# Kernel tuning notes

Hardware: AMD Instinct MI355X
Metric: run time of the kernel (lower is better)

## Reference

```python
import jax, jax.numpy as jnp
import numpy as np

B, S, D, H = 2, 2048, 1024, 16
HSZ = D // H  # 64


def setup_inputs() -> dict:
    key = jax.random.key(0)
    k0, k1, k2, k3, k4 = jax.random.split(key, 5)
    scale = 0.02
    return {
        "x": jax.random.normal(k0, (B, S, D), dtype=jnp.float32),
        "in_proj_w": jax.random.normal(k1, (3 * D, D), dtype=jnp.float32) * scale,
        "in_proj_b": jax.random.normal(k2, (3 * D,), dtype=jnp.float32) * scale,
        "out_proj_w": jax.random.normal(k3, (D, D), dtype=jnp.float32) * scale,
        "out_proj_b": jax.random.normal(k4, (D,), dtype=jnp.float32) * scale,
    }


def reference(x, in_proj_w, in_proj_b, out_proj_w, out_proj_b):
    # Packed QKV projection (self-attention fast path: query is key is value).
    qkv = x @ in_proj_w.T + in_proj_b              # (B, S, 3D)
    q, k, v = jnp.split(qkv, 3, axis=-1)           # each (B, S, D)

    def to_heads(t):
        return t.reshape(B, S, H, HSZ).transpose(0, 2, 1, 3)  # (B, H, S, hsz)

    q, k, v = to_heads(q), to_heads(k), to_heads(v)

    # Causal additive bias: -inf above the diagonal (tril keeps, logical_not masks).
    neg_inf = jnp.float32(-jnp.inf)
    causal = jnp.tril(jnp.ones((S, S), dtype=bool))
    attn_bias = jnp.where(causal, jnp.float32(0.0), neg_inf)  # (S, S)

    inv_sqrt = jnp.float32(1.0 / np.sqrt(HSZ))
    scores = jnp.einsum("bhqd,bhkd->bhqk", q * inv_sqrt, k) + attn_bias
    attn_w = jax.nn.softmax(scores, axis=-1)       # (B, H, S, S)

    out = jnp.einsum("bhqk,bhkd->bhqd", attn_w, v)  # (B, H, S, hsz)
    out = jnp.nan_to_num(out, nan=0.0)              # matches torch.nan_to_num_
    out = out.transpose(0, 2, 1, 3).reshape(B, S, D)  # concat heads
    out = out @ out_proj_w.T + out_proj_b           # (B, S, D)
    return out, attn_w
```

## Files before the change

kernel.cpp:

```cpp
#include <hip/hip_runtime.h>
#include <stdint.h>

typedef __bf16 bf16;
typedef __attribute__((ext_vector_type(8))) __bf16 bf16x8;
typedef __attribute__((ext_vector_type(4))) __bf16 bf16x4;
typedef __attribute__((ext_vector_type(4))) float f32x4;

#define MFMA16(a, b, c) __builtin_amdgcn_mfma_f32_16x16x32_bf16((a), (b), (c), 0, 0, 0)

constexpr int S = 2048, Dm = 1024, HS = 64;
constexpr float SCALE = 0.125f;
constexpr float SHIFT = 8.0f;

__device__ __forceinline__ int ktmax_of(int qt) { return (qt * 64 + 191) >> 7; }

__device__ __forceinline__ void job_decode(int j, int& qt, int& kg) {
  int acc = 0;
  for (int q = 0; q < 32; ++q) {
    const int ng = (ktmax_of(q) + 3) >> 2;
    if (j < acc + ng) { qt = q; kg = j - acc; return; }
    acc += ng;
  }
  qt = 31; kg = 0;
}

__device__ __forceinline__ void gld_lds16(const void* g, void* lds_uniform) {
  __builtin_amdgcn_global_load_lds(
      (const __attribute__((address_space(1))) void*)g,
      (__attribute__((address_space(3))) void*)lds_uniform,
      16, 0, 0);
}

__global__ __launch_bounds__(256) void cvt_kernel(const float* __restrict__ src,
                                                  bf16* __restrict__ dst, int n) {
  int i4 = (blockIdx.x * 256 + threadIdx.x) * 4;
  if (i4 < n) {
    const float4 f = *(const float4*)(src + i4);
    bf16x4 o;
    o[0] = (bf16)f.x; o[1] = (bf16)f.y; o[2] = (bf16)f.z; o[3] = (bf16)f.w;
    *(bf16x4*)(dst + i4) = o;
  }
}

__global__ __launch_bounds__(256) void gemm_bt_kernel(
    const bf16* __restrict__ A, const bf16* __restrict__ Bw,
    const float* __restrict__ bias, void* __restrict__ Cout,
    int N, int K, int out_is_bf16) {
  __shared__ bf16 As[128 * 32];
  __shared__ bf16 Bs[128 * 32];
  const int t = threadIdx.x;
  const int wave = t >> 6, lane = t & 63, quad = lane >> 4, l15 = lane & 15;
  const int wm = wave >> 1, wn = wave & 1;
  const int m0 = blockIdx.y * 128, n0 = blockIdx.x * 128;

  f32x4 acc[4][4];
#pragma unroll
  for (int mt = 0; mt < 4; ++mt)
#pragma unroll
    for (int nt = 0; nt < 4; ++nt) acc[mt][nt] = f32x4{0.f, 0.f, 0.f, 0.f};

  const bf16* Ag = A + (size_t)(m0 + (t >> 2)) * K + (t & 3) * 8;
  const bf16* Bg = Bw + (size_t)(n0 + (t >> 2)) * K + (t & 3) * 8;
  char* AsB = (char*)As;
  char* BsB = (char*)Bs;
  const int woff = wave * 1024;

  for (int k0 = 0; k0 < K; k0 += 32) {
    __syncthreads();
    gld_lds16(Ag + k0, AsB + woff);
    gld_lds16(Ag + (size_t)64 * K + k0, AsB + 4096 + woff);
    gld_lds16(Bg + k0, BsB + woff);
    gld_lds16(Bg + (size_t)64 * K + k0, BsB + 4096 + woff);
    __syncthreads();
    bf16x8 af[4], bfr[4];
#pragma unroll
    for (int mt = 0; mt < 4; ++mt)
      af[mt] = *(const bf16x8*)(As + (wm * 64 + mt * 16 + l15) * 32 + quad * 8);
#pragma unroll
    for (int nt = 0; nt < 4; ++nt)
      bfr[nt] = *(const bf16x8*)(Bs + (wn * 64 + nt * 16 + l15) * 32 + quad * 8);
#pragma unroll
    for (int mt = 0; mt < 4; ++mt)
#pragma unroll
      for (int nt = 0; nt < 4; ++nt)
        acc[mt][nt] = MFMA16(af[mt], bfr[nt], acc[mt][nt]);
  }

#pragma unroll
  for (int mt = 0; mt < 4; ++mt) {
    const int row = m0 + wm * 64 + mt * 16 + quad * 4;
#pragma unroll
    for (int nt = 0; nt < 4; ++nt) {
      const int col = n0 + wn * 64 + nt * 16 + l15;
      const float bcol = bias[col];
#pragma unroll
      for (int r = 0; r < 4; ++r) {
        float v = acc[mt][nt][r] + bcol;
        if (out_is_bf16)
          ((bf16*)Cout)[(size_t)(row + r) * N + col] = (bf16)v;
        else
          ((float*)Cout)[(size_t)(row + r) * N + col] = v;
      }
    }
  }
}

__global__ __launch_bounds__(256) void gemm_bt64_kernel(
    const bf16* __restrict__ A, const bf16* __restrict__ Bw,
    const float* __restrict__ bias, float* __restrict__ Cout,
    int N, int K) {
  __shared__ bf16 As[64 * 32];
  __shared__ bf16 Bs[128 * 32];
  const int t = threadIdx.x;
  const int wave = t >> 6, lane = t & 63, quad = lane >> 4, l15 = lane & 15;
  const int wm = wave >> 1, wn = wave & 1;
  const int m0 = blockIdx.y * 64, n0 = blockIdx.x * 128;

  f32x4 acc[2][4];
#pragma unroll
  for (int mt = 0; mt < 2; ++mt)
#pragma unroll
    for (int nt = 0; nt < 4; ++nt) acc[mt][nt] = f32x4{0.f, 0.f, 0.f, 0.f};

  const bf16* Ag = A + (size_t)(m0 + (t >> 2)) * K + (t & 3) * 8;
  const bf16* Bg = Bw + (size_t)(n0 + (t >> 2)) * K + (t & 3) * 8;
  char* AsB = (char*)As;
  char* BsB = (char*)Bs;
  const int woff = wave * 1024;

  for (int k0 = 0; k0 < K; k0 += 32) {
    __syncthreads();
    gld_lds16(Ag + k0, AsB + woff);
    gld_lds16(Bg + k0, BsB + woff);
    gld_lds16(Bg + (size_t)64 * K + k0, BsB + 4096 + woff);
    __syncthreads();
    bf16x8 af[2], bfr[4];
#pragma unroll
    for (int mt = 0; mt < 2; ++mt)
      af[mt] = *(const bf16x8*)(As + (wm * 32 + mt * 16 + l15) * 32 + quad * 8);
#pragma unroll
    for (int nt = 0; nt < 4; ++nt)
      bfr[nt] = *(const bf16x8*)(Bs + (wn * 64 + nt * 16 + l15) * 32 + quad * 8);
#pragma unroll
    for (int mt = 0; mt < 2; ++mt)
#pragma unroll
      for (int nt = 0; nt < 4; ++nt)
        acc[mt][nt] = MFMA16(af[mt], bfr[nt], acc[mt][nt]);
  }

#pragma unroll
  for (int mt = 0; mt < 2; ++mt) {
    const int row = m0 + wm * 32 + mt * 16 + quad * 4;
#pragma unroll
    for (int nt = 0; nt < 4; ++nt) {
      const int col = n0 + wn * 64 + nt * 16 + l15;
      const float bcol = bias[col];
#pragma unroll
      for (int r = 0; r < 4; ++r)
        Cout[(size_t)(row + r) * N + col] = acc[mt][nt][r] + bcol;
    }
  }
}

__global__ __launch_bounds__(256) void stats_kernel(const bf16* __restrict__ qkv,
                                                    float* __restrict__ lsum) {
  const int t = threadIdx.x, wave = t >> 6, lane = t & 63, quad = lane >> 4, l15 = lane & 15;
  int qt, kg;
  job_decode(79 - blockIdx.x, qt, kg);
  const int bh = blockIdx.y, b = bh >> 4, h = bh & 15;
  const int q0 = qt * 64;

  const bf16* qbase = qkv + (size_t)b * S * (3 * Dm) + h * HS;
  const bf16* kbase = qbase + Dm;
  const bf16* qrow = qbase + (size_t)(q0 + wave * 16 + l15) * (3 * Dm);
  const bf16x8 qf0 = *(const bf16x8*)(qrow + quad * 8);
  const bf16x8 qf1 = *(const bf16x8*)(qrow + 32 + quad * 8);
  const int rowb = q0 + wave * 16 + quad * 4;

  const int kt0 = kg * 4, kt1 = min(kt0 + 4, ktmax_of(qt));
  float accr[4] = {0.f, 0.f, 0.f, 0.f};

  for (int kt = kt0; kt < kt1; ++kt) {
    const int kc0 = kt * 128;
    f32x4 sacc[8];
#pragma unroll
    for (int nt = 0; nt < 8; ++nt) sacc[nt] = f32x4{0.f, 0.f, 0.f, 0.f};
#pragma unroll
    for (int nt = 0; nt < 8; ++nt) {
      const bf16* krow = kbase + (size_t)(kc0 + nt * 16 + l15) * (3 * Dm);
      const bf16x8 kf0 = *(const bf16x8*)(krow + quad * 8);
      const bf16x8 kf1 = *(const bf16x8*)(krow + 32 + quad * 8);
      sacc[nt] = MFMA16(qf0, kf0, sacc[nt]);
      sacc[nt] = MFMA16(qf1, kf1, sacc[nt]);
    }
#pragma unroll
    for (int nt = 0; nt < 8; ++nt) {
      const int col = kc0 + nt * 16 + l15;
#pragma unroll
      for (int r = 0; r < 4; ++r) {
        if (col <= rowb + r) accr[r] += __expf(sacc[nt][r] * SCALE - SHIFT);
      }
    }
  }
#pragma unroll
  for (int r = 0; r < 4; ++r) {
    float v = accr[r];
#pragma unroll
    for (int off = 1; off < 16; off <<= 1) v += __shfl_xor(v, off, 16);
    if (l15 == 0) atomicAdd(&lsum[bh * S + rowb + r], v);
  }
}

__global__ __launch_bounds__(256) void write_pv_kernel(
    const bf16* __restrict__ qkv, const float* __restrict__ lsum,
    float* __restrict__ attnw, float* __restrict__ Oacc) {
  constexpr int PSF = 132;
  constexpr int VST = 136;
  __shared__ float Ps[64 * PSF];
  __shared__ bf16 Vt[64 * VST];
  const int t = threadIdx.x, wave = t >> 6, lane = t & 63, quad = lane >> 4, l15 = lane & 15;
  int qt, kg;
  job_decode(79 - blockIdx.x, qt, kg);
  const int bh = blockIdx.y, b = bh >> 4, h = bh & 15;
  const int q0 = qt * 64;

  const bf16* qbase = qkv + (size_t)b * S * (3 * Dm) + h * HS;
  const bf16* kbase = qbase + Dm;
  const bf16* vbase = qbase + 2 * Dm;
  const bf16* qrow = qbase + (size_t)(q0 + wave * 16 + l15) * (3 * Dm);
  const bf16x8 qf0 = *(const bf16x8*)(qrow + quad * 8);
  const bf16x8 qf1 = *(const bf16x8*)(qrow + 32 + quad * 8);
  const int rowb = q0 + wave * 16 + quad * 4;

  float rl[4];
#pragma unroll
  for (int r = 0; r < 4; ++r) rl[r] = 1.f / lsum[bh * S + rowb + r];

  f32x4 oacc[4];
#pragma unroll
  for (int nto = 0; nto < 4; ++nto) oacc[nto] = f32x4{0.f, 0.f, 0.f, 0.f};

  float* aw = attnw + ((size_t)bh * S + q0) * S;
  const int kt0 = kg * 4, kt1 = min(kt0 + 4, ktmax_of(qt));

  for (int kt = kt0; kt < kt1; ++kt) {
    const int kc0 = kt * 128;
    __syncthreads();
    {
      ushort* vt = (ushort*)Vt;
#pragma unroll
      for (int it = 0; it < 16; ++it) {
        const int idx = it * 512 + t * 2;
        const int key = idx >> 6, hd = idx & 63;
        const unsigned u =
            *(const unsigned*)(vbase + (size_t)(kc0 + key) * (3 * Dm) + hd);
        vt[hd * VST + key] = (ushort)(u & 0xffffu);
        vt[(hd + 1) * VST + key] = (ushort)(u >> 16);
      }
    }
    f32x4 sacc[8];
#pragma unroll
    for (int nt = 0; nt < 8; ++nt) sacc[nt] = f32x4{0.f, 0.f, 0.f, 0.f};
#pragma unroll
    for (int nt = 0; nt < 8; ++nt) {
      const bf16* krow = kbase + (size_t)(kc0 + nt * 16 + l15) * (3 * Dm);
      const bf16x8 kf0 = *(const bf16x8*)(krow + quad * 8);
      const bf16x8 kf1 = *(const bf16x8*)(krow + 32 + quad * 8);
      sacc[nt] = MFMA16(qf0, kf0, sacc[nt]);
      sacc[nt] = MFMA16(qf1, kf1, sacc[nt]);
    }
#pragma unroll
    for (int nt = 0; nt < 8; ++nt) {
      const int col = kc0 + nt * 16 + l15;
#pragma unroll
      for (int r = 0; r < 4; ++r) {
        const float p = (col <= rowb + r)
                            ? __expf(sacc[nt][r] * SCALE - SHIFT) * rl[r]
                            : 0.f;
        Ps[(wave * 16 + quad * 4 + r) * PSF + nt * 16 + l15] = p;
      }
    }
    __syncthreads();

#pragma unroll
    for (int i = 0; i < 8; ++i) {
      const int idx = i * 256 + lane * 4;
      const int row16 = idx >> 7, col = idx & 127;
      const f32x4 v = *(const f32x4*)(Ps + (wave * 16 + row16) * PSF + col);
      __builtin_nontemporal_store(
          v, (f32x4*)(aw + (size_t)(wave * 16 + row16) * S + kc0 + col));
    }

#pragma unroll
    for (int ks = 0; ks < 4; ++ks) {
      const float* prow = Ps + (wave * 16 + l15) * PSF + ks * 32 + quad * 8;
      const f32x4 p0 = *(const f32x4*)prow;
      const f32x4 p1 = *(const f32x4*)(prow + 4);
      bf16x8 pa;
#pragma unroll
      for (int j = 0; j < 4; ++j) { pa[j] = (bf16)p0[j]; pa[4 + j] = (bf16)p1[j]; }
#pragma unroll
      for (int nto = 0; nto < 4; ++nto) {
        const bf16x8 vb =
            *(const bf16x8*)(Vt + (nto * 16 + l15) * VST + ks * 32 + quad * 8);
        oacc[nto] = MFMA16(pa, vb, oacc[nto]);
      }
    }
  }

#pragma unroll
  for (int nto = 0; nto < 4; ++nto) {
    const int hd = nto * 16 + l15;
#pragma unroll
    for (int r = 0; r < 4; ++r) {
      atomicAdd(&Oacc[((size_t)bh * S + rowb + r) * 64 + hd], oacc[nto][r]);
    }
  }
}

__global__ __launch_bounds__(256) void zf_kernel(float* __restrict__ attnw) {
  const int t = threadIdx.x;
  const int qt = blockIdx.x, bh = blockIdx.y;
  const int c0 = ktmax_of(qt) * 128;
  const int nv = (S - c0) >> 2;
  if (nv <= 0) return;
  float* aw = attnw + ((size_t)bh * S + qt * 64) * S + c0;
  const f32x4 z = {0.f, 0.f, 0.f, 0.f};
  for (int rr = 0; rr < 64; ++rr) {
    float* rowp = aw + (size_t)rr * S;
    for (int cc = t; cc < nv; cc += 256)
      __builtin_nontemporal_store(z, (f32x4*)(rowp + cc * 4));
  }
}

__global__ __launch_bounds__(256) void ocvt_kernel(const float* __restrict__ Oacc,
                                                   bf16* __restrict__ ho) {
  const int i4 = (blockIdx.x * 256 + threadIdx.x) * 4;
  const int bh = i4 >> 17, rem = i4 & 131071;
  const int row = rem >> 6, hd = rem & 63;
  const int b = bh >> 4, h = bh & 15;
  const float4 f = *(const float4*)(Oacc + i4);
  bf16x4 o;
  o[0] = (bf16)f.x; o[1] = (bf16)f.y; o[2] = (bf16)f.z; o[3] = (bf16)f.w;
  *(bf16x4*)(ho + (size_t)(b * S + row) * Dm + h * HS + hd) = o;
}

extern "C" void kernel_launch(void* const* d_in, const int* in_sizes, int n_in,
                              void* d_out, int out_size, void* d_ws, size_t ws_size,
                              hipStream_t stream) {
  (void)in_sizes; (void)n_in; (void)out_size; (void)ws_size;
  const float* x = (const float*)d_in[0];
  const float* wi = (const float*)d_in[1];
  const float* bi = (const float*)d_in[2];
  const float* wo = (const float*)d_in[3];
  const float* bo = (const float*)d_in[4];

  char* ws = (char*)d_ws;
  bf16* qkv = (bf16*)(ws);
  bf16* ho = (bf16*)(ws + 25165824);
  float* lsum = (float*)(ws + 25165824);
  float* Oacc = (float*)(ws + 33554432);
  bf16* xb = (bf16*)(ws + 33554432);
  bf16* wib = (bf16*)(ws + 41943040);
  bf16* wob = (bf16*)(ws);

  float* out = (float*)d_out;
  float* attnw = out + (size_t)4194304;

  cvt_kernel<<<4096, 256, 0, stream>>>(x, xb, 4194304);
  cvt_kernel<<<3072, 256, 0, stream>>>(wi, wib, 3145728);
  gemm_bt_kernel<<<dim3(24, 32), 256, 0, stream>>>(xb, wib, bi, qkv, 3072, 1024, 1);
  hipMemsetAsync(Oacc, 0, 16777216, stream);
  hipMemsetAsync(lsum, 0, 262144, stream);
  stats_kernel<<<dim3(80, 32), 256, 0, stream>>>(qkv, lsum);
  write_pv_kernel<<<dim3(80, 32), 256, 0, stream>>>(qkv, lsum, attnw, Oacc);
  zf_kernel<<<dim3(32, 32), 256, 0, stream>>>(attnw);
  cvt_kernel<<<1024, 256, 0, stream>>>(wo, wob, 1048576);
  ocvt_kernel<<<4096, 256, 0, stream>>>(Oacc, ho);
  gemm_bt64_kernel<<<dim3(8, 64), 256, 0, stream>>>(ho, wob, bo, out, 1024, 1024);
}
```

Before: 845.0 us.

## Fuse stats, PV, zero-fill and output conversion into one attention kernel per query tile

Replaces the split-K stats and write/PV kernels, the zero-fill kernel, the fp32 O accumulator memsets and the output conversion kernel with one kernel. Each block owns a full 64-row query tile: it zero-fills the masked columns, computes the row sums over all key tiles, then writes probabilities and the PV product, storing bf16 head output directly. This removes the atomics, the memsets and several launches. In exchange the grid shrinks from 80x32 to 32x32 blocks, so work is unbalanced across causal tiles (up to 16 key tiles per block) and occupancy is lower.

```diff
diff --git a/kernel.cpp b/kernel.cpp
--- a/kernel.cpp
+++ b/kernel.cpp
@@ -13,16 +13,6 @@
 constexpr float SHIFT = 8.0f;
 
 __device__ __forceinline__ int ktmax_of(int qt) { return (qt * 64 + 191) >> 7; }
-
-__device__ __forceinline__ void job_decode(int j, int& qt, int& kg) {
-  int acc = 0;
-  for (int q = 0; q < 32; ++q) {
-    const int ng = (ktmax_of(q) + 3) >> 2;
-    if (j < acc + ng) { qt = q; kg = j - acc; return; }
-    acc += ng;
-  }
-  qt = 31; kg = 0;
-}
 
 __device__ __forceinline__ void gld_lds16(const void* g, void* lds_uniform) {
   __builtin_amdgcn_global_load_lds(
@@ -44,8 +34,8 @@
 
 __global__ __launch_bounds__(256) void gemm_bt_kernel(
     const bf16* __restrict__ A, const bf16* __restrict__ Bw,
-    const float* __restrict__ bias, void* __restrict__ Cout,
-    int N, int K, int out_is_bf16) {
+    const float* __restrict__ bias, bf16* __restrict__ Cout,
+    int N, int K) {
   __shared__ bf16 As[128 * 32];
   __shared__ bf16 Bs[128 * 32];
   const int t = threadIdx.x;
@@ -94,13 +84,8 @@
       const int col = n0 + wn * 64 + nt * 16 + l15;
       const float bcol = bias[col];
 #pragma unroll
-      for (int r = 0; r < 4; ++r) {
-        float v = acc[mt][nt][r] + bcol;
-        if (out_is_bf16)
-          ((bf16*)Cout)[(size_t)(row + r) * N + col] = (bf16)v;
-        else
-          ((float*)Cout)[(size_t)(row + r) * N + col] = v;
-      }
+      for (int r = 0; r < 4; ++r)
+        Cout[(size_t)(row + r) * N + col] = (bf16)(acc[mt][nt][r] + bcol);
     }
   }
 }
@@ -162,67 +147,18 @@
   }
 }
 
-__global__ __launch_bounds__(256) void stats_kernel(const bf16* __restrict__ qkv,
-                                                    float* __restrict__ lsum) {
-  const int t = threadIdx.x, wave = t >> 6, lane = t & 63, quad = lane >> 4, l15 = lane & 15;
-  int qt, kg;
-  job_decode(79 - blockIdx.x, qt, kg);
-  const int bh = blockIdx.y, b = bh >> 4, h = bh & 15;
-  const int q0 = qt * 64;
-
-  const bf16* qbase = qkv + (size_t)b * S * (3 * Dm) + h * HS;
-  const bf16* kbase = qbase + Dm;
-  const bf16* qrow = qbase + (size_t)(q0 + wave * 16 + l15) * (3 * Dm);
-  const bf16x8 qf0 = *(const bf16x8*)(qrow + quad * 8);
-  const bf16x8 qf1 = *(const bf16x8*)(qrow + 32 + quad * 8);
-  const int rowb = q0 + wave * 16 + quad * 4;
-
-  const int kt0 = kg * 4, kt1 = min(kt0 + 4, ktmax_of(qt));
-  float accr[4] = {0.f, 0.f, 0.f, 0.f};
-
-  for (int kt = kt0; kt < kt1; ++kt) {
-    const int kc0 = kt * 128;
-    f32x4 sacc[8];
-#pragma unroll
-    for (int nt = 0; nt < 8; ++nt) sacc[nt] = f32x4{0.f, 0.f, 0.f, 0.f};
-#pragma unroll
-    for (int nt = 0; nt < 8; ++nt) {
-      const bf16* krow = kbase + (size_t)(kc0 + nt * 16 + l15) * (3 * Dm);
-      const bf16x8 kf0 = *(const bf16x8*)(krow + quad * 8);
-      const bf16x8 kf1 = *(const bf16x8*)(krow + 32 + quad * 8);
-      sacc[nt] = MFMA16(qf0, kf0, sacc[nt]);
-      sacc[nt] = MFMA16(qf1, kf1, sacc[nt]);
-    }
-#pragma unroll
-    for (int nt = 0; nt < 8; ++nt) {
-      const int col = kc0 + nt * 16 + l15;
-#pragma unroll
-      for (int r = 0; r < 4; ++r) {
-        if (col <= rowb + r) accr[r] += __expf(sacc[nt][r] * SCALE - SHIFT);
-      }
-    }
-  }
-#pragma unroll
-  for (int r = 0; r < 4; ++r) {
-    float v = accr[r];
-#pragma unroll
-    for (int off = 1; off < 16; off <<= 1) v += __shfl_xor(v, off, 16);
-    if (l15 == 0) atomicAdd(&lsum[bh * S + rowb + r], v);
-  }
-}
-
-__global__ __launch_bounds__(256) void write_pv_kernel(
-    const bf16* __restrict__ qkv, const float* __restrict__ lsum,
-    float* __restrict__ attnw, float* __restrict__ Oacc) {
+__global__ __launch_bounds__(256) void attn_fused_kernel(
+    const bf16* __restrict__ qkv, float* __restrict__ attnw,
+    bf16* __restrict__ ho) {
   constexpr int PSF = 132;
   constexpr int VST = 136;
   __shared__ float Ps[64 * PSF];
   __shared__ bf16 Vt[64 * VST];
   const int t = threadIdx.x, wave = t >> 6, lane = t & 63, quad = lane >> 4, l15 = lane & 15;
-  int qt, kg;
-  job_decode(79 - blockIdx.x, qt, kg);
+  const int qt = 31 - blockIdx.x;
   const int bh = blockIdx.y, b = bh >> 4, h = bh & 15;
   const int q0 = qt * 64;
+  const int ktmax = ktmax_of(qt);
 
   const bf16* qbase = qkv + (size_t)b * S * (3 * Dm) + h * HS;
   const bf16* kbase = qbase + Dm;
@@ -232,18 +168,58 @@
   const bf16x8 qf1 = *(const bf16x8*)(qrow + 32 + quad * 8);
   const int rowb = q0 + wave * 16 + quad * 4;
 
+  float* aw = attnw + ((size_t)bh * S + q0) * S;
+
+  {
+    const int c0 = ktmax * 128;
+    const int nv = (S - c0) >> 2;
+    if (nv > 0) {
+      const f32x4 z = {0.f, 0.f, 0.f, 0.f};
+      for (int rr = 0; rr < 64; ++rr) {
+        float* rowp = aw + (size_t)rr * S + c0;
+        for (int cc = t; cc < nv; cc += 256)
+          __builtin_nontemporal_store(z, (f32x4*)(rowp + cc * 4));
+      }
+    }
+  }
+
+  float accr[4] = {0.f, 0.f, 0.f, 0.f};
+  for (int kt = 0; kt < ktmax; ++kt) {
+    const int kc0 = kt * 128;
+    f32x4 sacc[8];
+#pragma unroll
+    for (int nt = 0; nt < 8; ++nt) sacc[nt] = f32x4{0.f, 0.f, 0.f, 0.f};
+#pragma unroll
+    for (int nt = 0; nt < 8; ++nt) {
+      const bf16* krow = kbase + (size_t)(kc0 + nt * 16 + l15) * (3 * Dm);
+      const bf16x8 kf0 = *(const bf16x8*)(krow + quad * 8);
+      const bf16x8 kf1 = *(const bf16x8*)(krow + 32 + quad * 8);
+      sacc[nt] = MFMA16(qf0, kf0, sacc[nt]);
+      sacc[nt] = MFMA16(qf1, kf1, sacc[nt]);
+    }
+#pragma unroll
+    for (int nt = 0; nt < 8; ++nt) {
+      const int col = kc0 + nt * 16 + l15;
+#pragma unroll
+      for (int r = 0; r < 4; ++r) {
+        if (col <= rowb + r) accr[r] += __expf(sacc[nt][r] * SCALE - SHIFT);
+      }
+    }
+  }
   float rl[4];
 #pragma unroll
-  for (int r = 0; r < 4; ++r) rl[r] = 1.f / lsum[bh * S + rowb + r];
+  for (int r = 0; r < 4; ++r) {
+    float v = accr[r];
+#pragma unroll
+    for (int off = 1; off < 16; off <<= 1) v += __shfl_xor(v, off, 16);
+    rl[r] = 1.f / v;
+  }
 
   f32x4 oacc[4];
 #pragma unroll
   for (int nto = 0; nto < 4; ++nto) oacc[nto] = f32x4{0.f, 0.f, 0.f, 0.f};
 
-  float* aw = attnw + ((size_t)bh * S + q0) * S;
-  const int kt0 = kg * 4, kt1 = min(kt0 + 4, ktmax_of(qt));
-
-  for (int kt = kt0; kt < kt1; ++kt) {
+  for (int kt = 0; kt < ktmax; ++kt) {
     const int kc0 = kt * 128;
     __syncthreads();
     {
@@ -313,36 +289,9 @@
     const int hd = nto * 16 + l15;
 #pragma unroll
     for (int r = 0; r < 4; ++r) {
-      atomicAdd(&Oacc[((size_t)bh * S + rowb + r) * 64 + hd], oacc[nto][r]);
-    }
-  }
-}
-
-__global__ __launch_bounds__(256) void zf_kernel(float* __restrict__ attnw) {
-  const int t = threadIdx.x;
-  const int qt = blockIdx.x, bh = blockIdx.y;
-  const int c0 = ktmax_of(qt) * 128;
-  const int nv = (S - c0) >> 2;
-  if (nv <= 0) return;
-  float* aw = attnw + ((size_t)bh * S + qt * 64) * S + c0;
-  const f32x4 z = {0.f, 0.f, 0.f, 0.f};
-  for (int rr = 0; rr < 64; ++rr) {
-    float* rowp = aw + (size_t)rr * S;
-    for (int cc = t; cc < nv; cc += 256)
-      __builtin_nontemporal_store(z, (f32x4*)(rowp + cc * 4));
-  }
-}
-
-__global__ __launch_bounds__(256) void ocvt_kernel(const float* __restrict__ Oacc,
-                                                   bf16* __restrict__ ho) {
-  const int i4 = (blockIdx.x * 256 + threadIdx.x) * 4;
-  const int bh = i4 >> 17, rem = i4 & 131071;
-  const int row = rem >> 6, hd = rem & 63;
-  const int b = bh >> 4, h = bh & 15;
-  const float4 f = *(const float4*)(Oacc + i4);
-  bf16x4 o;
-  o[0] = (bf16)f.x; o[1] = (bf16)f.y; o[2] = (bf16)f.z; o[3] = (bf16)f.w;
-  *(bf16x4*)(ho + (size_t)(b * S + row) * Dm + h * HS + hd) = o;
+      ho[(size_t)(b * S + rowb + r) * Dm + h * HS + hd] = (bf16)oacc[nto][r];
+    }
+  }
 }
 
 extern "C" void kernel_launch(void* const* d_in, const int* in_sizes, int n_in,
@@ -358,24 +307,17 @@
   char* ws = (char*)d_ws;
   bf16* qkv = (bf16*)(ws);
   bf16* ho = (bf16*)(ws + 25165824);
-  float* lsum = (float*)(ws + 25165824);
-  float* Oacc = (float*)(ws + 33554432);
   bf16* xb = (bf16*)(ws + 33554432);
   bf16* wib = (bf16*)(ws + 41943040);
-  bf16* wob = (bf16*)(ws);
+  bf16* wob = (bf16*)(ws + 33554432);
 
   float* out = (float*)d_out;
   float* attnw = out + (size_t)4194304;
 
   cvt_kernel<<<4096, 256, 0, stream>>>(x, xb, 4194304);
   cvt_kernel<<<3072, 256, 0, stream>>>(wi, wib, 3145728);
-  gemm_bt_kernel<<<dim3(24, 32), 256, 0, stream>>>(xb, wib, bi, qkv, 3072, 1024, 1);
-  hipMemsetAsync(Oacc, 0, 16777216, stream);
-  hipMemsetAsync(lsum, 0, 262144, stream);
-  stats_kernel<<<dim3(80, 32), 256, 0, stream>>>(qkv, lsum);
-  write_pv_kernel<<<dim3(80, 32), 256, 0, stream>>>(qkv, lsum, attnw, Oacc);
-  zf_kernel<<<dim3(32, 32), 256, 0, stream>>>(attnw);
+  gemm_bt_kernel<<<dim3(24, 32), 256, 0, stream>>>(xb, wib, bi, qkv, 3072, 1024);
+  attn_fused_kernel<<<dim3(32, 32), 256, 0, stream>>>(qkv, attnw, ho);
   cvt_kernel<<<1024, 256, 0, stream>>>(wo, wob, 1048576);
-  ocvt_kernel<<<4096, 256, 0, stream>>>(Oacc, ho);
   gemm_bt64_kernel<<<dim3(8, 64), 256, 0, stream>>>(ho, wob, bo, out, 1024, 1024);
 }
```

New measurement: 914.4 us. +8.2%, slower.
